# Performance work log

Measured on AMD Instinct MI355X. Metric: run time of the kernel, lower is better.

Reference implementation:

```python
import jax, jax.numpy as jnp
import numpy as np
import math

NUM_BLOCKS = 8
SPARSITY_THRESHOLD = 0.01
HARD_FRAC = 1.0
HIDDEN_SIZE = 1024
HIDDEN_FACTOR = 2
SCALE = 0.02


def _dht1d(x, axis):
    # Discrete Hartley transform along `axis`: sum x * cas(2*pi*k*n/N)
    # cas = cos + sin, equivalently Re(FFT) - Im(FFT).
    F = jnp.fft.fft(x, axis=axis)
    return F.real - F.imag


def dht2d(x):
    # Separable 2D Hartley transform over the spatial axes (1, 2) of (B,H,W,C).
    return _dht1d(_dht1d(x, 1), 2)


def setup_inputs() -> dict:
    key = jax.random.key(0)
    k_x, k_w1, k_b1, k_w2, k_b2 = jax.random.split(key, 5)
    B, N, C = 4, 16384, HIDDEN_SIZE
    bs = C // NUM_BLOCKS                      # 128
    hid = bs * HIDDEN_FACTOR                  # 256
    x = jax.random.normal(k_x, (B, N, C), dtype=jnp.float32)
    w1 = SCALE * jax.random.normal(k_w1, (2, NUM_BLOCKS, bs, hid), dtype=jnp.float32)
    b1 = SCALE * jax.random.normal(k_b1, (2, NUM_BLOCKS, hid), dtype=jnp.float32)
    w2 = SCALE * jax.random.normal(k_w2, (2, NUM_BLOCKS, hid, bs), dtype=jnp.float32)
    b2 = SCALE * jax.random.normal(k_b2, (2, NUM_BLOCKS, bs), dtype=jnp.float32)
    return {"x": x, "w1": w1, "b1": b1, "w2": w2, "b2": b2}


def reference(x, w1, b1, w2, b2):
    bias = x
    B, N, C = x.shape
    H = W = int(math.sqrt(N))
    bs = C // NUM_BLOCKS

    xs = x.reshape(B, H, W, C)
    xs = dht2d(xs)                                    # spatial Hartley domain
    xs = xs.reshape(B, H, W, NUM_BLOCKS, bs)

    kept = int(math.sqrt(H * W) * HARD_FRAC)          # = H when frac == 1
    xk = xs[:, :kept, :kept]                          # (B, kept, kept, nb, bs)

    # Block-diagonal spectral MLP; the source sums contributions from both
    # weight slices w[0] and w[1] with bias b[0].
    o1 = jax.nn.relu(
        jnp.einsum("bxyni,nio->bxyno", xk, w1[0])
        + jnp.einsum("bxyni,nio->bxyno", xk, w1[1])
        + b1[0]
    )                                                 # (B, kept, kept, nb, hid)
    o2k = (
        jnp.einsum("bxyno,noi->bxyni", o1, w2[0])
        + jnp.einsum("bxyno,noi->bxyni", o1, w2[1])
        + b2[0]
    )                                                 # (B, kept, kept, nb, bs)

    o2 = jnp.zeros_like(xs).at[:, :kept, :kept].set(o2k)

    # softshrink
    lam = jnp.float32(SPARSITY_THRESHOLD)
    z = jnp.sign(o2) * jax.nn.relu(jnp.abs(o2) - lam)

    z = z.reshape(B, H, W, C)
    z = dht2d(z) / (H * W)                            # inverse Hartley
    return z.reshape(B, N, C) + bias
```

## Files before the change

kernel.cpp:

```cpp
#include <hip/hip_runtime.h>

typedef unsigned short u16;
typedef unsigned int   u32;
typedef __attribute__((ext_vector_type(8))) short bf16x8;
typedef __attribute__((ext_vector_type(4))) short bf16x4;
typedef __attribute__((ext_vector_type(4))) float f32x4;

#define LAM 0.01f

__device__ __forceinline__ u16 f2bf(float f){
  u32 u = __float_as_uint(f);
  u = u + 0x7FFFu + ((u >> 16) & 1u);
  return (u16)(u >> 16);
}

__device__ __forceinline__ int swz(int row, int k){
  return row*128 + ((((k >> 3) ^ row) & 15) << 3) + (k & 7);
}

#define MFMA16(ac, a, b) ac = __builtin_amdgcn_mfma_f32_16x16x32_bf16((a), (b), (ac), 0, 0, 0)

#define GEMM_STEP(acc, A0,A1,A2,A3, B0,B1,B2,B3) \
  MFMA16(acc[0], A0,B0); MFMA16(acc[1], A0,B1); MFMA16(acc[2], A0,B2); MFMA16(acc[3], A0,B3); \
  MFMA16(acc[4], A1,B0); MFMA16(acc[5], A1,B1); MFMA16(acc[6], A1,B2); MFMA16(acc[7], A1,B3); \
  MFMA16(acc[8], A2,B0); MFMA16(acc[9], A2,B1); MFMA16(acc[10],A2,B2); MFMA16(acc[11],A2,B3); \
  MFMA16(acc[12],A3,B0); MFMA16(acc[13],A3,B1); MFMA16(acc[14],A3,B2); MFMA16(acc[15],A3,B3);

__global__ void k_prep(const float* __restrict__ w1, const float* __restrict__ w2,
                       u16* __restrict__ Mg, u16* __restrict__ W1et, u16* __restrict__ W2et){
  int gid = blockIdx.x * 256 + threadIdx.x;
  if (gid < 16384){
    int i = gid >> 7, j = gid & 127;
    int t = (i * j) & 127;
    float ang = (float)t * 0.04908738521234052f;
    Mg[gid] = f2bf(cosf(ang) + sinf(ang));
  } else if (gid < 16384 + 262144){
    int e = gid - 16384;
    int n = e >> 15, o = (e >> 7) & 255, i = e & 127;
    float v = w1[(n*128 + i)*256 + o] + w1[((8+n)*128 + i)*256 + o];
    W1et[e] = f2bf(v);
  } else {
    int e = gid - (16384 + 262144);
    int n = e >> 15, i = (e >> 8) & 127, o = e & 255;
    float v = w2[(n*256 + o)*128 + i] + w2[((8+n)*256 + o)*128 + i];
    W2et[e] = f2bf(v);
  }
}

__launch_bounds__(256, 4)
__global__ void k_dht_fwd(const float* __restrict__ x, const u16* __restrict__ Mg,
                          u16* __restrict__ Ag){
  __shared__ u16 xt[128*128];
  int bi = blockIdx.x;
  int n = bi & 7, w = (bi >> 3) & 127, b = bi >> 10;
  int tid = threadIdx.x;
  int lane = tid & 63, wid = tid >> 6;
  int l15 = lane & 15, q = lane >> 4;
  int r0 = (wid >> 1) * 64, c0 = (wid & 1) * 64;

  {
    int c = tid & 127, hg = tid >> 7;
    const float* xb = x + ((b*128)*128 + w)*1024 + n*128 + c;
    for (int it = 0; it < 32; ++it){
      int h0 = (hg + 2*it) * 2;
      float v0 = __builtin_nontemporal_load(xb + h0 * 131072);
      float v1 = __builtin_nontemporal_load(xb + (h0+1) * 131072);
      u32 pk = (u32)f2bf(v0) | ((u32)f2bf(v1) << 16);
      *(u32*)(&xt[swz(c, h0)]) = pk;
    }
  }
  __syncthreads();

  f32x4 acc[16];
#pragma unroll
  for (int t = 0; t < 16; ++t) acc[t] = f32x4{0.f,0.f,0.f,0.f};

#pragma unroll
  for (int ks = 0; ks < 4; ++ks){
    int kk = ks*32 + q*8;
    bf16x8 a0 = *(const bf16x8*)(Mg + (r0 +  0 + l15)*128 + kk);
    bf16x8 a1 = *(const bf16x8*)(Mg + (r0 + 16 + l15)*128 + kk);
    bf16x8 a2 = *(const bf16x8*)(Mg + (r0 + 32 + l15)*128 + kk);
    bf16x8 a3 = *(const bf16x8*)(Mg + (r0 + 48 + l15)*128 + kk);
    bf16x8 b0 = *(const bf16x8*)(&xt[swz(c0 +  0 + l15, kk)]);
    bf16x8 b1 = *(const bf16x8*)(&xt[swz(c0 + 16 + l15, kk)]);
    bf16x8 b2 = *(const bf16x8*)(&xt[swz(c0 + 32 + l15, kk)]);
    bf16x8 b3 = *(const bf16x8*)(&xt[swz(c0 + 48 + l15, kk)]);
    GEMM_STEP(acc, a0,a1,a2,a3, b0,b1,b2,b3);
  }
  __syncthreads();

#pragma unroll
  for (int i = 0; i < 4; ++i){
    int rb = r0 + 16*i + q*4;
#pragma unroll
    for (int j = 0; j < 4; ++j){
      int col = c0 + 16*j + l15;
      f32x4 v = acc[i*4+j];
      xt[swz(rb+0, col)] = f2bf(v.x);
      xt[swz(rb+1, col)] = f2bf(v.y);
      xt[swz(rb+2, col)] = f2bf(v.z);
      xt[swz(rb+3, col)] = f2bf(v.w);
    }
  }
  __syncthreads();
  u16* Aout = Ag + ((b*128)*128 + w)*1024 + n*128;
#pragma unroll
  for (int it = 0; it < 8; ++it){
    int cid = it*256 + tid;
    int row = cid >> 4, cp = cid & 15;
    bf16x8 v = *(const bf16x8*)(&xt[row*128 + (((cp ^ row) & 15) << 3)]);
    __builtin_nontemporal_store(v, (bf16x8*)(Aout + row*131072 + cp*8));
  }
}

__launch_bounds__(256, 2)
__global__ void k_mlp(const u16* __restrict__ Xg, const u16* __restrict__ W1et,
                      const u16* __restrict__ W2et, const u16* __restrict__ Mg,
                      const float* __restrict__ b1g, const float* __restrict__ b2g,
                      u16* __restrict__ Ug){
  __shared__ u16 bufA[128*128];
  __shared__ u16 bufB[128*128];
  int bi = blockIdx.x;
  int n = bi & 7, h = (bi >> 3) & 127, b = bi >> 10;
  int tid = threadIdx.x;
  int lane = tid & 63, wid = tid >> 6;
  int l15 = lane & 15, q = lane >> 4;
  int r0 = (wid >> 1) * 64, c0 = (wid & 1) * 64;

  const u16*  Xbase  = Xg + ((b*128 + h)*128)*1024 + n*128;
  const u16*  W1base = W1et + n*256*128;
  const u16*  W2base = W2et + n*128*256;
  const float* b1base = b1g + n*256;
  const float* b2base = b2g + n*128;

  bf16x8 xa[16];
#pragma unroll
  for (int ks = 0; ks < 4; ++ks){
    int kk = ks*32 + q*8;
#pragma unroll
    for (int g = 0; g < 4; ++g)
      xa[ks*4+g] = *(const bf16x8*)(Xbase + (r0 + 16*g + l15)*1024 + kk);
  }

  f32x4 acc2[16], acc1[16];
#pragma unroll
  for (int t = 0; t < 16; ++t) acc2[t] = f32x4{0.f,0.f,0.f,0.f};

  for (int half = 0; half < 2; ++half){
#pragma unroll
    for (int t = 0; t < 16; ++t) acc1[t] = f32x4{0.f,0.f,0.f,0.f};
#pragma unroll
    for (int ks = 0; ks < 4; ++ks){
      int kk = ks*32 + q*8;
      const u16* wb = W1base + (half*128 + c0 + l15)*128 + kk;
      bf16x8 b0 = *(const bf16x8*)(wb);
      bf16x8 b1 = *(const bf16x8*)(wb + 16*128);
      bf16x8 b2 = *(const bf16x8*)(wb + 32*128);
      bf16x8 b3 = *(const bf16x8*)(wb + 48*128);
      GEMM_STEP(acc1, xa[ks*4+0], xa[ks*4+1], xa[ks*4+2], xa[ks*4+3], b0,b1,b2,b3);
    }
#pragma unroll
    for (int i = 0; i < 4; ++i){
      int kw = r0 + 16*i + q*4;
#pragma unroll
      for (int j = 0; j < 4; ++j){
        int row = c0 + 16*j + l15;
        f32x4 v = acc1[i*4+j];
        bf16x4 pk;
        pk.x = (short)f2bf(v.x); pk.y = (short)f2bf(v.y);
        pk.z = (short)f2bf(v.z); pk.w = (short)f2bf(v.w);
        *(bf16x4*)(&bufA[swz(row, kw)]) = pk;
      }
    }
    __syncthreads();

#pragma unroll
    for (int t = 0; t < 16; ++t) acc1[t] = f32x4{0.f,0.f,0.f,0.f};
#pragma unroll
    for (int ks = 0; ks < 4; ++ks){
      int kk = ks*32 + q*8;
      bf16x8 a0 = *(const bf16x8*)(&bufA[swz(r0 +  0 + l15, kk)]);
      bf16x8 a1 = *(const bf16x8*)(&bufA[swz(r0 + 16 + l15, kk)]);
      bf16x8 a2 = *(const bf16x8*)(&bufA[swz(r0 + 32 + l15, kk)]);
      bf16x8 a3 = *(const bf16x8*)(&bufA[swz(r0 + 48 + l15, kk)]);
      bf16x8 b0 = *(const bf16x8*)(Mg + (c0 +  0 + l15)*128 + kk);
      bf16x8 b1 = *(const bf16x8*)(Mg + (c0 + 16 + l15)*128 + kk);
      bf16x8 b2 = *(const bf16x8*)(Mg + (c0 + 32 + l15)*128 + kk);
      bf16x8 b3 = *(const bf16x8*)(Mg + (c0 + 48 + l15)*128 + kk);
      GEMM_STEP(acc1, a0,a1,a2,a3, b0,b1,b2,b3);
    }
#pragma unroll
    for (int i = 0; i < 4; ++i){
      int ko = r0 + 16*i + q*4;
      float bs0 = b1base[half*128 + ko + 0];
      float bs1 = b1base[half*128 + ko + 1];
      float bs2 = b1base[half*128 + ko + 2];
      float bs3 = b1base[half*128 + ko + 3];
#pragma unroll
      for (int j = 0; j < 4; ++j){
        int row = c0 + 16*j + l15;
        f32x4 v = acc1[i*4+j];
        bf16x4 pk;
        pk.x = (short)f2bf(fmaxf(v.x + bs0, 0.f));
        pk.y = (short)f2bf(fmaxf(v.y + bs1, 0.f));
        pk.z = (short)f2bf(fmaxf(v.z + bs2, 0.f));
        pk.w = (short)f2bf(fmaxf(v.w + bs3, 0.f));
        *(bf16x4*)(&bufB[swz(row, ko)]) = pk;
      }
    }
    __syncthreads();

#pragma unroll
    for (int ks = 0; ks < 4; ++ks){
      int kk = ks*32 + q*8;
      bf16x8 a0 = *(const bf16x8*)(&bufB[swz(r0 +  0 + l15, kk)]);
      bf16x8 a1 = *(const bf16x8*)(&bufB[swz(r0 + 16 + l15, kk)]);
      bf16x8 a2 = *(const bf16x8*)(&bufB[swz(r0 + 32 + l15, kk)]);
      bf16x8 a3 = *(const bf16x8*)(&bufB[swz(r0 + 48 + l15, kk)]);
      const u16* wb = W2base + (c0 + l15)*256 + half*128 + kk;
      bf16x8 b0 = *(const bf16x8*)(wb);
      bf16x8 b1 = *(const bf16x8*)(wb + 16*256);
      bf16x8 b2 = *(const bf16x8*)(wb + 32*256);
      bf16x8 b3 = *(const bf16x8*)(wb + 48*256);
      GEMM_STEP(acc2, a0,a1,a2,a3, b0,b1,b2,b3);
    }
    __syncthreads();
  }

  {
    float b2v[4];
#pragma unroll
    for (int j = 0; j < 4; ++j) b2v[j] = b2base[c0 + 16*j + l15];
#pragma unroll
    for (int i = 0; i < 4; ++i){
      int kw = r0 + 16*i + q*4;
#pragma unroll
      for (int j = 0; j < 4; ++j){
        int row = c0 + 16*j + l15;
        f32x4 v = acc2[i*4+j];
        float t0 = v.x + b2v[j], t1 = v.y + b2v[j], t2 = v.z + b2v[j], t3 = v.w + b2v[j];
        float m0 = fmaxf(fabsf(t0) - LAM, 0.f);
        float m1 = fmaxf(fabsf(t1) - LAM, 0.f);
        float m2 = fmaxf(fabsf(t2) - LAM, 0.f);
        float m3 = fmaxf(fabsf(t3) - LAM, 0.f);
        bf16x4 pk;
        pk.x = (short)f2bf(t0 >= 0.f ? m0 : -m0);
        pk.y = (short)f2bf(t1 >= 0.f ? m1 : -m1);
        pk.z = (short)f2bf(t2 >= 0.f ? m2 : -m2);
        pk.w = (short)f2bf(t3 >= 0.f ? m3 : -m3);
        *(bf16x4*)(&bufA[swz(row, kw)]) = pk;
      }
    }
  }
  __syncthreads();

#pragma unroll
  for (int t = 0; t < 16; ++t) acc1[t] = f32x4{0.f,0.f,0.f,0.f};
#pragma unroll
  for (int ks = 0; ks < 4; ++ks){
    int kk = ks*32 + q*8;
    bf16x8 a0 = *(const bf16x8*)(Mg + (r0 +  0 + l15)*128 + kk);
    bf16x8 a1 = *(const bf16x8*)(Mg + (r0 + 16 + l15)*128 + kk);
    bf16x8 a2 = *(const bf16x8*)(Mg + (r0 + 32 + l15)*128 + kk);
    bf16x8 a3 = *(const bf16x8*)(Mg + (r0 + 48 + l15)*128 + kk);
    bf16x8 b0 = *(const bf16x8*)(&bufA[swz(c0 +  0 + l15, kk)]);
    bf16x8 b1 = *(const bf16x8*)(&bufA[swz(c0 + 16 + l15, kk)]);
    bf16x8 b2 = *(const bf16x8*)(&bufA[swz(c0 + 32 + l15, kk)]);
    bf16x8 b3 = *(const bf16x8*)(&bufA[swz(c0 + 48 + l15, kk)]);
    GEMM_STEP(acc1, a0,a1,a2,a3, b0,b1,b2,b3);
  }
#pragma unroll
  for (int i = 0; i < 4; ++i){
    int rb = r0 + 16*i + q*4;
#pragma unroll
    for (int j = 0; j < 4; ++j){
      int col = c0 + 16*j + l15;
      f32x4 v = acc1[i*4+j];
      bufB[swz(rb+0, col)] = f2bf(v.x);
      bufB[swz(rb+1, col)] = f2bf(v.y);
      bufB[swz(rb+2, col)] = f2bf(v.z);
      bufB[swz(rb+3, col)] = f2bf(v.w);
    }
  }
  __syncthreads();
  u16* Ubase = Ug + ((b*128 + h)*128)*1024 + n*128;
#pragma unroll
  for (int it = 0; it < 8; ++it){
    int cid = it*256 + tid;
    int row = cid >> 4, cp = cid & 15;
    bf16x8 v = *(const bf16x8*)(&bufB[row*128 + (((cp ^ row) & 15) << 3)]);
    __builtin_nontemporal_store(v, (bf16x8*)(Ubase + row*1024 + cp*8));
  }
}

__launch_bounds__(256, 4)
__global__ void k_dht_inv(const u16* __restrict__ Ug, const u16* __restrict__ Mg,
                          const float* __restrict__ x, float* __restrict__ out){
  __shared__ u16 ut[128*128];
  int bi = blockIdx.x;
  int n = bi & 7, w = (bi >> 3) & 127, b = bi >> 10;
  int tid = threadIdx.x;
  int lane = tid & 63, wid = tid >> 6;
  int l15 = lane & 15, q = lane >> 4;
  int r0 = (wid >> 1) * 64, c0 = (wid & 1) * 64;

  {
    int cp = (tid & 63) * 2, hb = (tid >> 6) * 2;
    const u16* Ub = Ug + ((b*128)*128 + w)*1024 + n*128;
#pragma unroll
    for (int it = 0; it < 16; ++it){
      int h0 = hb + it*8;
      u32 d0 = __builtin_nontemporal_load((const u32*)(Ub + h0*131072 + cp));
      u32 d1 = __builtin_nontemporal_load((const u32*)(Ub + (h0+1)*131072 + cp));
      u32 lo = (d0 & 0xFFFFu) | ((d1 & 0xFFFFu) << 16);
      u32 hi = (d0 >> 16) | (d1 & 0xFFFF0000u);
      *(u32*)(&ut[swz(cp,   h0)]) = lo;
      *(u32*)(&ut[swz(cp+1, h0)]) = hi;
    }
  }
  __syncthreads();

  f32x4 acc[16];
#pragma unroll
  for (int t = 0; t < 16; ++t) acc[t] = f32x4{0.f,0.f,0.f,0.f};

#pragma unroll
  for (int ks = 0; ks < 4; ++ks){
    int kk = ks*32 + q*8;
    bf16x8 a0 = *(const bf16x8*)(Mg + (r0 +  0 + l15)*128 + kk);
    bf16x8 a1 = *(const bf16x8*)(Mg + (r0 + 16 + l15)*128 + kk);
    bf16x8 a2 = *(const bf16x8*)(Mg + (r0 + 32 + l15)*128 + kk);
    bf16x8 a3 = *(const bf16x8*)(Mg + (r0 + 48 + l15)*128 + kk);
    bf16x8 b0 = *(const bf16x8*)(&ut[swz(c0 +  0 + l15, kk)]);
    bf16x8 b1 = *(const bf16x8*)(&ut[swz(c0 + 16 + l15, kk)]);
    bf16x8 b2 = *(const bf16x8*)(&ut[swz(c0 + 32 + l15, kk)]);
    bf16x8 b3 = *(const bf16x8*)(&ut[swz(c0 + 48 + l15, kk)]);
    GEMM_STEP(acc, a0,a1,a2,a3, b0,b1,b2,b3);
  }

  const float s = 1.f / 16384.f;
  int gbase = ((b*128)*128 + w)*1024 + n*128;
#pragma unroll
  for (int i = 0; i < 4; ++i){
    int hh = r0 + 16*i + q*4;
#pragma unroll
    for (int j = 0; j < 4; ++j){
      int cc = c0 + 16*j + l15;
      f32x4 v = acc[i*4+j];
      int i0 = gbase + (hh+0)*131072 + cc;
      int i1 = gbase + (hh+1)*131072 + cc;
      int i2 = gbase + (hh+2)*131072 + cc;
      int i3 = gbase + (hh+3)*131072 + cc;
      float x0 = __builtin_nontemporal_load(x + i0);
      float x1 = __builtin_nontemporal_load(x + i1);
      float x2 = __builtin_nontemporal_load(x + i2);
      float x3 = __builtin_nontemporal_load(x + i3);
      __builtin_nontemporal_store(v.x * s + x0, out + i0);
      __builtin_nontemporal_store(v.y * s + x1, out + i1);
      __builtin_nontemporal_store(v.z * s + x2, out + i2);
      __builtin_nontemporal_store(v.w * s + x3, out + i3);
    }
  }
}

extern "C" void kernel_launch(void* const* d_in, const int* in_sizes, int n_in,
                              void* d_out, int out_size, void* d_ws, size_t ws_size,
                              hipStream_t stream) {
  const float* x  = (const float*)d_in[0];
  const float* w1 = (const float*)d_in[1];
  const float* b1 = (const float*)d_in[2];
  const float* w2 = (const float*)d_in[3];
  const float* b2 = (const float*)d_in[4];
  float* out = (float*)d_out;

  u16* Ag   = (u16*)d_out;
  u16* W1et = (u16*)((char*)d_out + 267386880);
  u16* W2et = (u16*)((char*)d_out + 267911168);
  u16* Ug   = (u16*)d_ws;
  u16* Mg   = (u16*)((char*)d_ws + 134217728);

  k_prep<<<2112, 256, 0, stream>>>(w1, w2, Mg, W1et, W2et);
  k_dht_fwd<<<4096, 256, 0, stream>>>(x, Mg, Ag);
  k_mlp<<<4096, 256, 0, stream>>>(Ag, W1et, W2et, Mg, b1, b2, Ug);
  k_dht_inv<<<4096, 256, 0, stream>>>(Ug, Mg, x, out);
}
```

Before: 1.072 ms.

## Split k_mlp across 8 waves with smaller per-wave tiles and shared X staging

Doubles the k_mlp workgroup to 512 threads, giving each wave a 64x32 output tile instead of 64x64. This halves accumulator registers and is meant to raise occupancy and latency hiding. The X tile is now staged into LDS once with nontemporal loads instead of being held in registers per wave, and the two LDS buffers are merged into one reused buffer. The price is extra barriers between phases and more LDS reads per MFMA.

```diff
diff --git a/kernel.cpp b/kernel.cpp
--- a/kernel.cpp
+++ b/kernel.cpp
@@ -25,6 +25,12 @@
   MFMA16(acc[4], A1,B0); MFMA16(acc[5], A1,B1); MFMA16(acc[6], A1,B2); MFMA16(acc[7], A1,B3); \
   MFMA16(acc[8], A2,B0); MFMA16(acc[9], A2,B1); MFMA16(acc[10],A2,B2); MFMA16(acc[11],A2,B3); \
   MFMA16(acc[12],A3,B0); MFMA16(acc[13],A3,B1); MFMA16(acc[14],A3,B2); MFMA16(acc[15],A3,B3);
+
+#define GEMM_STEP42(acc, A0,A1,A2,A3, B0,B1) \
+  MFMA16(acc[0], A0,B0); MFMA16(acc[1], A0,B1); \
+  MFMA16(acc[2], A1,B0); MFMA16(acc[3], A1,B1); \
+  MFMA16(acc[4], A2,B0); MFMA16(acc[5], A2,B1); \
+  MFMA16(acc[6], A3,B0); MFMA16(acc[7], A3,B1);
 
 __global__ void k_prep(const float* __restrict__ w1, const float* __restrict__ w2,
                        u16* __restrict__ Mg, u16* __restrict__ W1et, u16* __restrict__ W2et){
@@ -114,19 +120,20 @@
   }
 }
 
-__launch_bounds__(256, 2)
+__launch_bounds__(512, 4)
 __global__ void k_mlp(const u16* __restrict__ Xg, const u16* __restrict__ W1et,
                       const u16* __restrict__ W2et, const u16* __restrict__ Mg,
                       const float* __restrict__ b1g, const float* __restrict__ b2g,
                       u16* __restrict__ Ug){
-  __shared__ u16 bufA[128*128];
-  __shared__ u16 bufB[128*128];
+  __shared__ u16 Xt[128*128];
+  __shared__ u16 buf[128*128];
   int bi = blockIdx.x;
   int n = bi & 7, h = (bi >> 3) & 127, b = bi >> 10;
   int tid = threadIdx.x;
   int lane = tid & 63, wid = tid >> 6;
   int l15 = lane & 15, q = lane >> 4;
-  int r0 = (wid >> 1) * 64, c0 = (wid & 1) * 64;
+  int r0 = (wid >> 2) * 64;
+  int c0 = (wid & 3) * 32;
 
   const u16*  Xbase  = Xg + ((b*128 + h)*128)*1024 + n*128;
   const u16*  W1base = W1et + n*256*128;
@@ -134,62 +141,66 @@
   const float* b1base = b1g + n*256;
   const float* b2base = b2g + n*128;
 
-  bf16x8 xa[16];
-#pragma unroll
-  for (int ks = 0; ks < 4; ++ks){
-    int kk = ks*32 + q*8;
-#pragma unroll
-    for (int g = 0; g < 4; ++g)
-      xa[ks*4+g] = *(const bf16x8*)(Xbase + (r0 + 16*g + l15)*1024 + kk);
-  }
-
-  f32x4 acc2[16], acc1[16];
-#pragma unroll
-  for (int t = 0; t < 16; ++t) acc2[t] = f32x4{0.f,0.f,0.f,0.f};
+  {
+    int c16 = tid & 15, rbase = tid >> 4;
+#pragma unroll
+    for (int it = 0; it < 4; ++it){
+      int r = rbase + it*32;
+      bf16x8 v = __builtin_nontemporal_load((const bf16x8*)(Xbase + r*1024 + c16*8));
+      *(bf16x8*)(&Xt[swz(r, c16*8)]) = v;
+    }
+  }
+  __syncthreads();
+
+  f32x4 acc2[8], acc1[8];
+#pragma unroll
+  for (int t = 0; t < 8; ++t) acc2[t] = f32x4{0.f,0.f,0.f,0.f};
 
   for (int half = 0; half < 2; ++half){
 #pragma unroll
-    for (int t = 0; t < 16; ++t) acc1[t] = f32x4{0.f,0.f,0.f,0.f};
+    for (int t = 0; t < 8; ++t) acc1[t] = f32x4{0.f,0.f,0.f,0.f};
 #pragma unroll
     for (int ks = 0; ks < 4; ++ks){
       int kk = ks*32 + q*8;
+      bf16x8 a0 = *(const bf16x8*)(&Xt[swz(r0 +  0 + l15, kk)]);
+      bf16x8 a1 = *(const bf16x8*)(&Xt[swz(r0 + 16 + l15, kk)]);
+      bf16x8 a2 = *(const bf16x8*)(&Xt[swz(r0 + 32 + l15, kk)]);
+      bf16x8 a3 = *(const bf16x8*)(&Xt[swz(r0 + 48 + l15, kk)]);
       const u16* wb = W1base + (half*128 + c0 + l15)*128 + kk;
       bf16x8 b0 = *(const bf16x8*)(wb);
       bf16x8 b1 = *(const bf16x8*)(wb + 16*128);
-      bf16x8 b2 = *(const bf16x8*)(wb + 32*128);
-      bf16x8 b3 = *(const bf16x8*)(wb + 48*128);
-      GEMM_STEP(acc1, xa[ks*4+0], xa[ks*4+1], xa[ks*4+2], xa[ks*4+3], b0,b1,b2,b3);
-    }
+      GEMM_STEP42(acc1, a0,a1,a2,a3, b0,b1);
+    }
+    __syncthreads();
 #pragma unroll
     for (int i = 0; i < 4; ++i){
       int kw = r0 + 16*i + q*4;
 #pragma unroll
-      for (int j = 0; j < 4; ++j){
+      for (int j = 0; j < 2; ++j){
         int row = c0 + 16*j + l15;
-        f32x4 v = acc1[i*4+j];
+        f32x4 v = acc1[i*2+j];
         bf16x4 pk;
         pk.x = (short)f2bf(v.x); pk.y = (short)f2bf(v.y);
         pk.z = (short)f2bf(v.z); pk.w = (short)f2bf(v.w);
-        *(bf16x4*)(&bufA[swz(row, kw)]) = pk;
+        *(bf16x4*)(&buf[swz(row, kw)]) = pk;
       }
     }
     __syncthreads();
 
 #pragma unroll
-    for (int t = 0; t < 16; ++t) acc1[t] = f32x4{0.f,0.f,0.f,0.f};
+    for (int t = 0; t < 8; ++t) acc1[t] = f32x4{0.f,0.f,0.f,0.f};
 #pragma unroll
     for (int ks = 0; ks < 4; ++ks){
       int kk = ks*32 + q*8;
-      bf16x8 a0 = *(const bf16x8*)(&bufA[swz(r0 +  0 + l15, kk)]);
-      bf16x8 a1 = *(const bf16x8*)(&bufA[swz(r0 + 16 + l15, kk)]);
-      bf16x8 a2 = *(const bf16x8*)(&bufA[swz(r0 + 32 + l15, kk)]);
-      bf16x8 a3 = *(const bf16x8*)(&bufA[swz(r0 + 48 + l15, kk)]);
+      bf16x8 a0 = *(const bf16x8*)(&buf[swz(r0 +  0 + l15, kk)]);
+      bf16x8 a1 = *(const bf16x8*)(&buf[swz(r0 + 16 + l15, kk)]);
+      bf16x8 a2 = *(const bf16x8*)(&buf[swz(r0 + 32 + l15, kk)]);
+      bf16x8 a3 = *(const bf16x8*)(&buf[swz(r0 + 48 + l15, kk)]);
       bf16x8 b0 = *(const bf16x8*)(Mg + (c0 +  0 + l15)*128 + kk);
       bf16x8 b1 = *(const bf16x8*)(Mg + (c0 + 16 + l15)*128 + kk);
-      bf16x8 b2 = *(const bf16x8*)(Mg + (c0 + 32 + l15)*128 + kk);
-      bf16x8 b3 = *(const bf16x8*)(Mg + (c0 + 48 + l15)*128 + kk);
-      GEMM_STEP(acc1, a0,a1,a2,a3, b0,b1,b2,b3);
-    }
+      GEMM_STEP42(acc1, a0,a1,a2,a3, b0,b1);
+    }
+    __syncthreads();
 #pragma unroll
     for (int i = 0; i < 4; ++i){
       int ko = r0 + 16*i + q*4;
@@ -198,15 +209,15 @@
       float bs2 = b1base[half*128 + ko + 2];
       float bs3 = b1base[half*128 + ko + 3];
 #pragma unroll
-      for (int j = 0; j < 4; ++j){
+      for (int j = 0; j < 2; ++j){
         int row = c0 + 16*j + l15;
-        f32x4 v = acc1[i*4+j];
+        f32x4 v = acc1[i*2+j];
         bf16x4 pk;
         pk.x = (short)f2bf(fmaxf(v.x + bs0, 0.f));
         pk.y = (short)f2bf(fmaxf(v.y + bs1, 0.f));
         pk.z = (short)f2bf(fmaxf(v.z + bs2, 0.f));
         pk.w = (short)f2bf(fmaxf(v.w + bs3, 0.f));
-        *(bf16x4*)(&bufB[swz(row, ko)]) = pk;
+        *(bf16x4*)(&buf[swz(row, ko)]) = pk;
       }
     }
     __syncthreads();
@@ -214,32 +225,30 @@
 #pragma unroll
     for (int ks = 0; ks < 4; ++ks){
       int kk = ks*32 + q*8;
-      bf16x8 a0 = *(const bf16x8*)(&bufB[swz(r0 +  0 + l15, kk)]);
-      bf16x8 a1 = *(const bf16x8*)(&bufB[swz(r0 + 16 + l15, kk)]);
-      bf16x8 a2 = *(const bf16x8*)(&bufB[swz(r0 + 32 + l15, kk)]);
-      bf16x8 a3 = *(const bf16x8*)(&bufB[swz(r0 + 48 + l15, kk)]);
+      bf16x8 a0 = *(const bf16x8*)(&buf[swz(r0 +  0 + l15, kk)]);
+      bf16x8 a1 = *(const bf16x8*)(&buf[swz(r0 + 16 + l15, kk)]);
+      bf16x8 a2 = *(const bf16x8*)(&buf[swz(r0 + 32 + l15, kk)]);
+      bf16x8 a3 = *(const bf16x8*)(&buf[swz(r0 + 48 + l15, kk)]);
       const u16* wb = W2base + (c0 + l15)*256 + half*128 + kk;
       bf16x8 b0 = *(const bf16x8*)(wb);
       bf16x8 b1 = *(const bf16x8*)(wb + 16*256);
-      bf16x8 b2 = *(const bf16x8*)(wb + 32*256);
-      bf16x8 b3 = *(const bf16x8*)(wb + 48*256);
-      GEMM_STEP(acc2, a0,a1,a2,a3, b0,b1,b2,b3);
+      GEMM_STEP42(acc2, a0,a1,a2,a3, b0,b1);
     }
     __syncthreads();
   }
 
   {
-    float b2v[4];
-#pragma unroll
-    for (int j = 0; j < 4; ++j) b2v[j] = b2base[c0 + 16*j + l15];
+    float b2v0 = b2base[c0 +  0 + l15];
+    float b2v1 = b2base[c0 + 16 + l15];
 #pragma unroll
     for (int i = 0; i < 4; ++i){
       int kw = r0 + 16*i + q*4;
 #pragma unroll
-      for (int j = 0; j < 4; ++j){
+      for (int j = 0; j < 2; ++j){
         int row = c0 + 16*j + l15;
-        f32x4 v = acc2[i*4+j];
-        float t0 = v.x + b2v[j], t1 = v.y + b2v[j], t2 = v.z + b2v[j], t3 = v.w + b2v[j];
+        float bb = j ? b2v1 : b2v0;
+        f32x4 v = acc2[i*2+j];
+        float t0 = v.x + bb, t1 = v.y + bb, t2 = v.z + bb, t3 = v.w + bb;
         float m0 = fmaxf(fabsf(t0) - LAM, 0.f);
         float m1 = fmaxf(fabsf(t1) - LAM, 0.f);
         float m2 = fmaxf(fabsf(t2) - LAM, 0.f);
@@ -249,14 +258,14 @@
         pk.y = (short)f2bf(t1 >= 0.f ? m1 : -m1);
         pk.z = (short)f2bf(t2 >= 0.f ? m2 : -m2);
         pk.w = (short)f2bf(t3 >= 0.f ? m3 : -m3);
-        *(bf16x4*)(&bufA[swz(row, kw)]) = pk;
+        *(bf16x4*)(&buf[swz(row, kw)]) = pk;
       }
     }
   }
   __syncthreads();
 
 #pragma unroll
-  for (int t = 0; t < 16; ++t) acc1[t] = f32x4{0.f,0.f,0.f,0.f};
+  for (int t = 0; t < 8; ++t) acc1[t] = f32x4{0.f,0.f,0.f,0.f};
 #pragma unroll
   for (int ks = 0; ks < 4; ++ks){
     int kk = ks*32 + q*8;
@@ -264,32 +273,31 @@
     bf16x8 a1 = *(const bf16x8*)(Mg + (r0 + 16 + l15)*128 + kk);
     bf16x8 a2 = *(const bf16x8*)(Mg + (r0 + 32 + l15)*128 + kk);
     bf16x8 a3 = *(const bf16x8*)(Mg + (r0 + 48 + l15)*128 + kk);
-    bf16x8 b0 = *(const bf16x8*)(&bufA[swz(c0 +  0 + l15, kk)]);
-    bf16x8 b1 = *(const bf16x8*)(&bufA[swz(c0 + 16 + l15, kk)]);
-    bf16x8 b2 = *(const bf16x8*)(&bufA[swz(c0 + 32 + l15, kk)]);
-    bf16x8 b3 = *(const bf16x8*)(&bufA[swz(c0 + 48 + l15, kk)]);
-    GEMM_STEP(acc1, a0,a1,a2,a3, b0,b1,b2,b3);
-  }
+    bf16x8 b0 = *(const bf16x8*)(&buf[swz(c0 +  0 + l15, kk)]);
+    bf16x8 b1 = *(const bf16x8*)(&buf[swz(c0 + 16 + l15, kk)]);
+    GEMM_STEP42(acc1, a0,a1,a2,a3, b0,b1);
+  }
+  __syncthreads();
 #pragma unroll
   for (int i = 0; i < 4; ++i){
     int rb = r0 + 16*i + q*4;
 #pragma unroll
-    for (int j = 0; j < 4; ++j){
+    for (int j = 0; j < 2; ++j){
       int col = c0 + 16*j + l15;
-      f32x4 v = acc1[i*4+j];
-      bufB[swz(rb+0, col)] = f2bf(v.x);
-      bufB[swz(rb+1, col)] = f2bf(v.y);
-      bufB[swz(rb+2, col)] = f2bf(v.z);
-      bufB[swz(rb+3, col)] = f2bf(v.w);
+      f32x4 v = acc1[i*2+j];
+      buf[swz(rb+0, col)] = f2bf(v.x);
+      buf[swz(rb+1, col)] = f2bf(v.y);
+      buf[swz(rb+2, col)] = f2bf(v.z);
+      buf[swz(rb+3, col)] = f2bf(v.w);
     }
   }
   __syncthreads();
   u16* Ubase = Ug + ((b*128 + h)*128)*1024 + n*128;
 #pragma unroll
-  for (int it = 0; it < 8; ++it){
-    int cid = it*256 + tid;
+  for (int it = 0; it < 4; ++it){
+    int cid = it*512 + tid;
     int row = cid >> 4, cp = cid & 15;
-    bf16x8 v = *(const bf16x8*)(&bufB[row*128 + (((cp ^ row) & 15) << 3)]);
+    bf16x8 v = *(const bf16x8*)(&buf[row*128 + (((cp ^ row) & 15) << 3)]);
     __builtin_nontemporal_store(v, (bf16x8*)(Ubase + row*1024 + cp*8));
   }
 }
@@ -382,6 +390,6 @@
 
   k_prep<<<2112, 256, 0, stream>>>(w1, w2, Mg, W1et, W2et);
   k_dht_fwd<<<4096, 256, 0, stream>>>(x, Mg, Ag);
-  k_mlp<<<4096, 256, 0, stream>>>(Ag, W1et, W2et, Mg, b1, b2, Ug);
+  k_mlp<<<4096, 512, 0, stream>>>(Ag, W1et, W2et, Mg, b1, b2, Ug);
   k_dht_inv<<<4096, 256, 0, stream>>>(Ug, Mg, x, out);
 }
```

New measurement: 989.3 us. 7.7% less time.
